# Performance work log

Measured on AMD Instinct MI355X. Metric: run time of the kernel, lower is better.

## Reference

```python
import jax, jax.numpy as jnp
import numpy as np

N = 256    # num_nodes = 2*K*R
K = 16     # num_cluster (after reflection pairing)
R = 8      # ratio = size of each original cluster
IN = 32
OUT = 32
BS = 32


def setup_inputs() -> dict:
    key = jax.random.key(0)
    k1, k2, k3, k4 = jax.random.split(key, 4)
    x = jax.random.normal(k1, (BS, N, IN), dtype=jnp.float32)
    w_diag = jax.random.uniform(k2, (IN * OUT, K), dtype=jnp.float32)           # torch.rand
    w_off = jax.random.uniform(k3, (IN * OUT, K, 2 * K), dtype=jnp.float32)     # torch.rand
    stdv = 1.0 / np.sqrt(OUT)
    b1 = jax.random.uniform(k4, (OUT,), minval=-stdv, maxval=stdv, dtype=jnp.float32)
    perm = np.random.default_rng(0).permutation(N)   # flatten_ids of shuffled clusters
    permute_ids = jnp.asarray(perm, dtype=jnp.int32)
    inv_permute = jnp.asarray(np.argsort(perm), dtype=jnp.int32)
    return {"x": x, "w_diag": w_diag, "w_off": w_off, "b1": b1,
            "permute_ids": permute_ids, "inv_permute": inv_permute}


def _build_W(w_diag, w_off):
    # Faithful to: kron(tie_weights(w_off), ones(R,R))/N + kron(diag_embed(repeat_interleave(w_diag,2)), eye(R))
    C = w_diag.shape[0]            # in*out channels
    width = 2 * K
    # tie_weights: interleave original rows with pair-swapped-column rows
    swap = np.arange(width).reshape(-1, 2)[:, ::-1].reshape(-1)      # [1,0,3,2,...]
    tied = jnp.stack([w_off, w_off[:, :, swap]], axis=2).reshape(C, width, width)
    # kron with ones(R,R) == repeat each entry R times along both node axes
    W3 = jnp.repeat(jnp.repeat(tied, R, axis=1), R, axis=2) / N      # (C, N, N)
    # kron(diag_embed(.), eye(R)) == add per-node diagonal, constant within cluster
    wd_full = jnp.repeat(jnp.repeat(w_diag, 2, axis=1), R, axis=1)   # (C, N)
    di = jnp.arange(N)
    W3 = W3.at[:, di, di].add(wd_full)
    # rearrange '(o i) j k -> (o j) (i k)'
    return W3.reshape(OUT, IN, N, N).transpose(0, 2, 1, 3).reshape(OUT * N, IN * N)


def reference(x, w_diag, w_off, b1, permute_ids, inv_permute):
    W = _build_W(w_diag, w_off)                       # (OUT*N, IN*N)
    xp = x[:, permute_ids, :]                         # (BS, N, IN) permuted
    xp = xp.transpose(0, 2, 1).reshape(BS, IN * N)    # feature-major flatten
    out = xp @ W.T                                    # (BS, OUT*N)
    out = out.reshape(BS, OUT, N).transpose(0, 2, 1)  # (BS, N, OUT)
    out = out[:, inv_permute, :] + b1[None, None, :]
    return out
```

## Files before the change

### kernel.cpp

```cpp
#include <hip/hip_runtime.h>

#define N_   256
#define IN_  32
#define OUT_ 32
#define BS_  32

__global__ __launch_bounds__(256) void k_yz(const float* __restrict__ x,
                                            const int* __restrict__ perm,
                                            const float* __restrict__ w_off,
                                            float* __restrict__ ws_z) {
    const int t = threadIdx.x;
    const int b = blockIdx.x;
    const int o  = b & 31;
    const int sg = b >> 5;
    const int u  = t & 15;
    const int i4 = (t >> 4) & 7;
    const int sh = t >> 7;

    __shared__ int   perm_s[256];
    __shared__ float y_lds[4 * 32 * 32];
    __shared__ float part[128][8];

    perm_s[t] = perm[t];

    float4 wv[4][8];
    const float* wbase = w_off + ((o * 32 + i4 * 4) * 16 + u) * 32;
#pragma unroll
    for (int di = 0; di < 4; ++di)
#pragma unroll
        for (int q4 = 0; q4 < 8; ++q4)
            wv[di][q4] = *(const float4*)(wbase + di * 512 + q4 * 4);

    __syncthreads();

    {
        const int i  = t & 31;
        const int qb = t >> 5;
#pragma unroll
        for (int sl = 0; sl < 4; ++sl) {
            const float* xs = x + (sg * 4 + sl) * (N_ * IN_);
#pragma unroll
            for (int k = 0; k < 4; ++k) {
                const int q = qb * 4 + k;
                float sum = 0.f;
#pragma unroll
                for (int j = 0; j < 8; ++j)
                    sum += xs[perm_s[8 * q + j] * IN_ + i];
                y_lds[sl * 1024 + q * 32 + i] = sum;
            }
        }
    }
    __syncthreads();

#define WEL(di, qq) (((const float*)&wv[di][(qq) >> 2])[(qq) & 3])

    float accs[2][2];
#pragma unroll
    for (int dsi = 0; dsi < 2; ++dsi) {
        const float* yb = y_lds + (sh * 2 + dsi) * 1024 + i4 * 4;
        float a0 = 0.f, a1 = 0.f;
#pragma unroll
        for (int q = 0; q < 32; ++q) {
            const float4 yv = *(const float4*)(yb + q * 32);
            const int q1 = q ^ 1;
            a0 += WEL(0, q)  * yv.x + WEL(1, q)  * yv.y + WEL(2, q)  * yv.z + WEL(3, q)  * yv.w;
            a1 += WEL(0, q1) * yv.x + WEL(1, q1) * yv.y + WEL(2, q1) * yv.z + WEL(3, q1) * yv.w;
        }
        accs[dsi][0] = a0;
        accs[dsi][1] = a1;
    }
#undef WEL

#pragma unroll
    for (int dsi = 0; dsi < 2; ++dsi)
#pragma unroll
        for (int p = 0; p < 2; ++p) {
            const int slot = ((sh * 2 + dsi) * 16 + u) * 2 + p;
            part[slot][i4] = accs[dsi][p];
        }
    __syncthreads();

    if (t < 128) {
        float sum = 0.f;
#pragma unroll
        for (int j = 0; j < 8; ++j) sum += part[t][j];
        const int s_local = t >> 5;
        const int uu = (t >> 1) & 15;
        const int pp = t & 1;
        const int s = sg * 4 + s_local;
        ws_z[((s * 32 + o) * 16 + uu) * 2 + pp] = sum * (1.0f / 256.0f);
    }
}

__global__ __launch_bounds__(256) void k_out(const float* __restrict__ x,
                                             const int* __restrict__ perm,
                                             const float* __restrict__ w_diag,
                                             const float* __restrict__ b1,
                                             const float* __restrict__ ws_z,
                                             float* __restrict__ out) {
    const int t = threadIdx.x;
    const int b = blockIdx.x;
    const int s = b >> 3;
    const int ac = b & 7;

    __shared__ float xrow[32 * 32];
    __shared__ float wdt[2][32 * 36];
    __shared__ float z_lds[1024];
    __shared__ int perm_lds[32];

    if (t < 32) perm_lds[t] = perm[ac * 32 + t];

    ((float4*)z_lds)[t] = ((const float4*)(ws_z + s * 1024))[t];

    {
        const int o = t >> 3;
        const int ii = (t & 7) * 4;
#pragma unroll
        for (int uu = 0; uu < 2; ++uu)
#pragma unroll
            for (int d = 0; d < 4; ++d)
                wdt[uu][o * 36 + ii + d] = w_diag[(o * 32 + ii + d) * 16 + ac * 2 + uu];
    }
    {
        const int r = t >> 3;
        const int col = (t & 7) * 4;
        const int rowp = perm[ac * 32 + r];
        const float4 v = *(const float4*)(x + (s * N_ + rowp) * IN_ + col);
        *(float4*)&xrow[r * 32 + col] = v;
    }
    __syncthreads();

    const int o = t & 31;
    const int rg = t >> 5;
    const int u_sel = rg >> 2;
    const int p = (rg >> 1) & 1;
    const int u = ac * 2 + u_sel;

    float4 wreg[8];
#pragma unroll
    for (int ii = 0; ii < 8; ++ii)
        wreg[ii] = *(const float4*)&wdt[u_sel][o * 36 + ii * 4];

    const float base = b1[o] + z_lds[(o * 16 + u) * 2 + p];

#pragma unroll
    for (int dr = 0; dr < 4; ++dr) {
        const int r = rg * 4 + dr;
        const float4* xr = (const float4*)&xrow[r * 32];
        float acc = base;
#pragma unroll
        for (int ii = 0; ii < 8; ++ii) {
            const float4 xv = xr[ii];
            const float4 wv = wreg[ii];
            acc += xv.x * wv.x + xv.y * wv.y + xv.z * wv.z + xv.w * wv.w;
        }
        out[(s * N_ + perm_lds[r]) * OUT_ + o] = acc;
    }
}

extern "C" void kernel_launch(void* const* d_in, const int* in_sizes, int n_in,
                              void* d_out, int out_size, void* d_ws, size_t ws_size,
                              hipStream_t stream) {
    const float* x      = (const float*)d_in[0];
    const float* w_diag = (const float*)d_in[1];
    const float* w_off  = (const float*)d_in[2];
    const float* b1     = (const float*)d_in[3];
    const int*   perm   = (const int*)d_in[4];

    float* out = (float*)d_out;
    float* ws_z = (float*)d_ws;

    k_yz<<<256, 256, 0, stream>>>(x, perm, w_off, ws_z);
    k_out<<<256, 256, 0, stream>>>(x, perm, w_diag, b1, ws_z, out);
}
```

Before: 75.82 us.

## Fuse cluster-sum and output kernels into one per-sample kernel

```diff
diff --git a/kernel.cpp b/kernel.cpp
--- a/kernel.cpp
+++ b/kernel.cpp
@@ -5,156 +5,124 @@
 #define OUT_ 32
 #define BS_  32
 
-__global__ __launch_bounds__(256) void k_yz(const float* __restrict__ x,
-                                            const int* __restrict__ perm,
-                                            const float* __restrict__ w_off,
-                                            float* __restrict__ ws_z) {
+__global__ __launch_bounds__(256) void k_fused(const float* __restrict__ x,
+                                               const int* __restrict__ perm,
+                                               const float* __restrict__ w_off,
+                                               const float* __restrict__ w_diag,
+                                               const float* __restrict__ b1,
+                                               float* __restrict__ out) {
     const int t = threadIdx.x;
     const int b = blockIdx.x;
-    const int o  = b & 31;
-    const int sg = b >> 5;
-    const int u  = t & 15;
-    const int i4 = (t >> 4) & 7;
-    const int sh = t >> 7;
+    const int s  = b >> 3;
+    const int og = b & 7;
 
     __shared__ int   perm_s[256];
-    __shared__ float y_lds[4 * 32 * 32];
-    __shared__ float part[128][8];
+    __shared__ float xp[256 * 36];
+    __shared__ float yT[32 * 36];
+    __shared__ float wdt[16 * 128];
+    __shared__ float part[128 * 5];
+    __shared__ float z_l[128];
 
     perm_s[t] = perm[t];
+    __syncthreads();
 
-    float4 wv[4][8];
-    const float* wbase = w_off + ((o * 32 + i4 * 4) * 16 + u) * 32;
+    {
+        const int r0 = t >> 3;
+        const int c  = (t & 7) * 4;
 #pragma unroll
-    for (int di = 0; di < 4; ++di)
+        for (int pass = 0; pass < 8; ++pass) {
+            const int r = pass * 32 + r0;
+            const float4 v = *(const float4*)(x + (s * N_ + perm_s[r]) * IN_ + c);
+            *(float4*)&xp[r * 36 + c] = v;
+        }
+    }
+    {
+        const int o_l = t >> 6;
+        const int i   = (t >> 1) & 31;
+        const int o   = og * 4 + o_l;
 #pragma unroll
-        for (int q4 = 0; q4 < 8; ++q4)
-            wv[di][q4] = *(const float4*)(wbase + di * 512 + q4 * 4);
-
+        for (int k = 0; k < 2; ++k) {
+            const int uq = (t & 1) * 2 + k;
+            const float4 v = *(const float4*)(w_diag + (o * 32 + i) * 16 + uq * 4);
+            wdt[(uq * 4 + 0) * 128 + o_l * 32 + i] = v.x;
+            wdt[(uq * 4 + 1) * 128 + o_l * 32 + i] = v.y;
+            wdt[(uq * 4 + 2) * 128 + o_l * 32 + i] = v.z;
+            wdt[(uq * 4 + 3) * 128 + o_l * 32 + i] = v.w;
+        }
+    }
     __syncthreads();
 
     {
         const int i  = t & 31;
         const int qb = t >> 5;
 #pragma unroll
-        for (int sl = 0; sl < 4; ++sl) {
-            const float* xs = x + (sg * 4 + sl) * (N_ * IN_);
+        for (int k = 0; k < 4; ++k) {
+            const int q = qb * 4 + k;
+            float sum = 0.f;
 #pragma unroll
-            for (int k = 0; k < 4; ++k) {
-                const int q = qb * 4 + k;
-                float sum = 0.f;
-#pragma unroll
-                for (int j = 0; j < 8; ++j)
-                    sum += xs[perm_s[8 * q + j] * IN_ + i];
-                y_lds[sl * 1024 + q * 32 + i] = sum;
-            }
+            for (int j = 0; j < 8; ++j)
+                sum += xp[(8 * q + j) * 36 + i];
+            yT[i * 36 + q] = sum;
         }
     }
     __syncthreads();
 
-#define WEL(di, qq) (((const float*)&wv[di][(qq) >> 2])[(qq) & 3])
-
-    float accs[2][2];
+    {
+        const int u   = t & 15;
+        const int o_l = (t >> 4) & 3;
+        const int qq  = t >> 6;
+        const int o   = og * 4 + o_l;
+        const float* wbase = w_off + ((o * 32) * 16 + u) * 32 + qq * 8;
+        const float* yb    = yT + qq * 8;
+        float p0 = 0.f, p1 = 0.f;
 #pragma unroll
-    for (int dsi = 0; dsi < 2; ++dsi) {
-        const float* yb = y_lds + (sh * 2 + dsi) * 1024 + i4 * 4;
-        float a0 = 0.f, a1 = 0.f;
-#pragma unroll
-        for (int q = 0; q < 32; ++q) {
-            const float4 yv = *(const float4*)(yb + q * 32);
-            const int q1 = q ^ 1;
-            a0 += WEL(0, q)  * yv.x + WEL(1, q)  * yv.y + WEL(2, q)  * yv.z + WEL(3, q)  * yv.w;
-            a1 += WEL(0, q1) * yv.x + WEL(1, q1) * yv.y + WEL(2, q1) * yv.z + WEL(3, q1) * yv.w;
+        for (int i = 0; i < 32; ++i) {
+            const float4 w0 = *(const float4*)(wbase + i * 512);
+            const float4 w1 = *(const float4*)(wbase + i * 512 + 4);
+            const float4 ya = *(const float4*)(yb + i * 36);
+            const float4 yc = *(const float4*)(yb + i * 36 + 4);
+            p0 += w0.x*ya.x + w0.y*ya.y + w0.z*ya.z + w0.w*ya.w
+                + w1.x*yc.x + w1.y*yc.y + w1.z*yc.z + w1.w*yc.w;
+            p1 += w0.y*ya.x + w0.x*ya.y + w0.w*ya.z + w0.z*ya.w
+                + w1.y*yc.x + w1.x*yc.y + w1.w*yc.z + w1.z*yc.w;
         }
-        accs[dsi][0] = a0;
-        accs[dsi][1] = a1;
+        const int slot = (o_l * 16 + u) * 2;
+        part[(slot + 0) * 5 + qq] = p0;
+        part[(slot + 1) * 5 + qq] = p1;
     }
-#undef WEL
-
-#pragma unroll
-    for (int dsi = 0; dsi < 2; ++dsi)
-#pragma unroll
-        for (int p = 0; p < 2; ++p) {
-            const int slot = ((sh * 2 + dsi) * 16 + u) * 2 + p;
-            part[slot][i4] = accs[dsi][p];
-        }
     __syncthreads();
 
     if (t < 128) {
-        float sum = 0.f;
-#pragma unroll
-        for (int j = 0; j < 8; ++j) sum += part[t][j];
-        const int s_local = t >> 5;
-        const int uu = (t >> 1) & 15;
-        const int pp = t & 1;
-        const int s = sg * 4 + s_local;
-        ws_z[((s * 32 + o) * 16 + uu) * 2 + pp] = sum * (1.0f / 256.0f);
-    }
-}
-
-__global__ __launch_bounds__(256) void k_out(const float* __restrict__ x,
-                                             const int* __restrict__ perm,
-                                             const float* __restrict__ w_diag,
-                                             const float* __restrict__ b1,
-                                             const float* __restrict__ ws_z,
-                                             float* __restrict__ out) {
-    const int t = threadIdx.x;
-    const int b = blockIdx.x;
-    const int s = b >> 3;
-    const int ac = b & 7;
-
-    __shared__ float xrow[32 * 32];
-    __shared__ float wdt[2][32 * 36];
-    __shared__ float z_lds[1024];
-    __shared__ int perm_lds[32];
-
-    if (t < 32) perm_lds[t] = perm[ac * 32 + t];
-
-    ((float4*)z_lds)[t] = ((const float4*)(ws_z + s * 1024))[t];
-
-    {
-        const int o = t >> 3;
-        const int ii = (t & 7) * 4;
-#pragma unroll
-        for (int uu = 0; uu < 2; ++uu)
-#pragma unroll
-            for (int d = 0; d < 4; ++d)
-                wdt[uu][o * 36 + ii + d] = w_diag[(o * 32 + ii + d) * 16 + ac * 2 + uu];
-    }
-    {
-        const int r = t >> 3;
-        const int col = (t & 7) * 4;
-        const int rowp = perm[ac * 32 + r];
-        const float4 v = *(const float4*)(x + (s * N_ + rowp) * IN_ + col);
-        *(float4*)&xrow[r * 32 + col] = v;
+        const float sum = part[t * 5 + 0] + part[t * 5 + 1]
+                        + part[t * 5 + 2] + part[t * 5 + 3];
+        const int o_l = t >> 5;
+        z_l[t] = sum * (1.0f / 256.0f) + b1[og * 4 + o_l];
     }
     __syncthreads();
 
-    const int o = t & 31;
-    const int rg = t >> 5;
-    const int u_sel = rg >> 2;
-    const int p = (rg >> 1) & 1;
-    const int u = ac * 2 + u_sel;
+    {
+        const int r = t;
+        const int u = r >> 4;
+        const int p = (r >> 3) & 1;
+        const float4* xr = (const float4*)&xp[r * 36];
+        float4 xv[8];
+#pragma unroll
+        for (int ii = 0; ii < 8; ++ii) xv[ii] = xr[ii];
 
-    float4 wreg[8];
+        float acc[4];
 #pragma unroll
-    for (int ii = 0; ii < 8; ++ii)
-        wreg[ii] = *(const float4*)&wdt[u_sel][o * 36 + ii * 4];
-
-    const float base = b1[o] + z_lds[(o * 16 + u) * 2 + p];
-
+        for (int o_l = 0; o_l < 4; ++o_l) {
+            float a = z_l[(o_l * 16 + u) * 2 + p];
+            const float4* wr = (const float4*)&wdt[u * 128 + o_l * 32];
 #pragma unroll
-    for (int dr = 0; dr < 4; ++dr) {
-        const int r = rg * 4 + dr;
-        const float4* xr = (const float4*)&xrow[r * 32];
-        float acc = base;
-#pragma unroll
-        for (int ii = 0; ii < 8; ++ii) {
-            const float4 xv = xr[ii];
-            const float4 wv = wreg[ii];
-            acc += xv.x * wv.x + xv.y * wv.y + xv.z * wv.z + xv.w * wv.w;
+            for (int ii = 0; ii < 8; ++ii) {
+                const float4 w = wr[ii];
+                a += xv[ii].x*w.x + xv[ii].y*w.y + xv[ii].z*w.z + xv[ii].w*w.w;
+            }
+            acc[o_l] = a;
         }
-        out[(s * N_ + perm_lds[r]) * OUT_ + o] = acc;
+        const float4 res = make_float4(acc[0], acc[1], acc[2], acc[3]);
+        *(float4*)(out + (s * N_ + perm_s[r]) * OUT_ + og * 4) = res;
     }
 }
 
@@ -168,8 +136,5 @@
     const int*   perm   = (const int*)d_in[4];
 
     float* out = (float*)d_out;
-    float* ws_z = (float*)d_ws;
-
-    k_yz<<<256, 256, 0, stream>>>(x, perm, w_off, ws_z);
-    k_out<<<256, 256, 0, stream>>>(x, perm, w_diag, b1, ws_z, out);
+    k_fused<<<256, 256, 0, stream>>>(x, perm, w_off, w_diag, b1, out);
 }
```

After: 74.83 us. About the same (-1.3%).
